# Kernel optimization log

Measured on AMD Instinct MI355X. Metric: run time of the kernel, lower is better.

Reference implementation:

```python
import jax, jax.numpy as jnp
import numpy as np

B, N_AIM, N_DET, C = 4, 2048, 2048, 256  # inplanes=256, inter_channels=128


def _lin(x, w, b):
    # torch nn.Linear: y = x @ W^T + b, weight shape [out, in]
    return jnp.einsum('bnc,dc->bnd', x, w) + b


def setup_inputs() -> dict:
    key = jax.random.key(0)
    ks = jax.random.split(key, 16)
    s = 1.0 / np.sqrt(C)
    inp = {
        'detect': jax.random.normal(ks[0], (B, N_DET, C), jnp.float32),
        'aim': jax.random.normal(ks[1], (B, N_AIM, C), jnp.float32),
    }
    names = ['g', 'g2', 'theta', 'phi', 'W', 'Q']
    for i, nm in enumerate(names):
        inp[nm + '_w'] = jax.random.uniform(ks[2 + 2 * i], (C, C), jnp.float32, -s, s)
        inp[nm + '_b'] = jax.random.uniform(ks[3 + 2 * i], (C,), jnp.float32, -s, s)
    return inp


def reference(detect, aim, g_w, g_b, g2_w, g2_b, theta_w, theta_b, phi_w, phi_b, W_w, W_b, Q_w, Q_b):
    b, na, c = aim.shape
    nd = detect.shape[1]
    ic = c // 2  # inter_channels

    # view(B, ic, -1) on a contiguous [B, N, C] tensor -> row-major reshape to [B, ic, 2N]
    d_x = _lin(detect, g_w, g_b).reshape(b, ic, -1).transpose(0, 2, 1)      # (B, 2Nd, ic)
    a_x = _lin(aim, g2_w, g2_b).reshape(b, ic, -1).transpose(0, 2, 1)       # (B, 2Na, ic)
    theta_x = _lin(aim, theta_w, theta_b).reshape(b, ic, -1).transpose(0, 2, 1)  # (B, 2Na, ic)
    phi_x = _lin(detect, phi_w, phi_b).reshape(b, ic, -1)                   # (B, ic, 2Nd)

    f = jnp.matmul(theta_x, phi_x)                 # (B, 2Na, 2Nd)
    f_div_C = f / f.shape[-1]                      # scale by 2*Nd
    fi_div_C = jnp.swapaxes(f, 1, 2) / f.shape[-2] # (B, 2Nd, 2Na), scale by 2*Na

    non_aim = jnp.matmul(f_div_C, d_x)             # (B, 2Na, ic)
    non_aim = non_aim.transpose(0, 2, 1).reshape(b, na, c)
    non_aim = _lin(non_aim, W_w, W_b) + aim

    non_det = jnp.matmul(fi_div_C, a_x)            # (B, 2Nd, ic)
    non_det = non_det.transpose(0, 2, 1).reshape(b, nd, c)
    non_det = _lin(non_det, Q_w, Q_b) + detect

    return (non_det, non_aim)
```

## Files before the change

### kernel.cpp

```cpp
#include <hip/hip_runtime.h>


typedef __attribute__((ext_vector_type(4))) float  f32x4;
typedef __attribute__((ext_vector_type(8))) __bf16 bf16x8;
typedef __attribute__((ext_vector_type(8))) unsigned short u16x8;
typedef __attribute__((ext_vector_type(4))) unsigned short u16x4;

__device__ inline unsigned short f2bf(float f) {
    union { float f; unsigned u; } c; c.f = f;
    unsigned r = c.u + 0x7FFF + ((c.u >> 16) & 1);
    return (unsigned short)(r >> 16);
}
__device__ inline bf16x8 ldfrag(const unsigned short* p) {
    return __builtin_bit_cast(bf16x8, *(const u16x8*)p);
}

struct Params {
    const float *detect, *aim;
    const float *g_w, *g2_w, *th_w, *ph_w, *W_w, *Q_w;
    const float *g_b, *g2_b, *th_b, *ph_b, *W_b, *Q_b;
    unsigned short *Wbf;
    unsigned short *T, *P, *Gd, *Ga;
    float *Spart;
    float *out_det, *out_aim;
};

__global__ __launch_bounds__(256)
void linall_kernel(Params p)
{
    const int z = blockIdx.z, set = blockIdx.x;
    const float* A  = z ? p.detect : p.aim;
    const float* Wm = z ? (set ? p.g_w : p.ph_w) : (set ? p.g2_w : p.th_w);
    const float* Bv = z ? (set ? p.g_b : p.ph_b) : (set ? p.g2_b : p.th_b);
    unsigned short* O = z ? (set ? p.Gd : p.P) : (set ? p.Ga : p.T);
    const int m0 = blockIdx.y * 128;

    __shared__ unsigned short As[128][40];
    __shared__ unsigned short Bs[256][40];

    const int tid = threadIdx.x, lane = tid & 63, w = tid >> 6;
    const int wr = w >> 1, wc = w & 1, q = lane >> 4, ln = lane & 15;

    f32x4 acc[4][8] = {};

    for (int k0 = 0; k0 < 256; k0 += 32) {
        #pragma unroll
        for (int i = 0; i < 4; ++i) {
            int c = tid + i * 256, row = c >> 3, c4 = c & 7;
            float4 v = *((const float4*)(A + (size_t)(m0 + row) * 256 + k0) + c4);
            u16x4 pk; pk[0]=f2bf(v.x); pk[1]=f2bf(v.y); pk[2]=f2bf(v.z); pk[3]=f2bf(v.w);
            *(u16x4*)&As[row][c4 * 4] = pk;
        }
        #pragma unroll
        for (int i = 0; i < 8; ++i) {
            int c = tid + i * 256, row = c >> 3, c4 = c & 7;
            float4 v = *((const float4*)(Wm + (size_t)row * 256 + k0) + c4);
            u16x4 pk; pk[0]=f2bf(v.x); pk[1]=f2bf(v.y); pk[2]=f2bf(v.z); pk[3]=f2bf(v.w);
            *(u16x4*)&Bs[row][c4 * 4] = pk;
        }
        __syncthreads();
        bf16x8 af[4], bb[8];
        #pragma unroll
        for (int i = 0; i < 4; ++i) af[i] = ldfrag(&As[wr * 64 + i * 16 + ln][q * 8]);
        #pragma unroll
        for (int j = 0; j < 8; ++j) bb[j] = ldfrag(&Bs[wc * 128 + j * 16 + ln][q * 8]);
        #pragma unroll
        for (int i = 0; i < 4; ++i)
            #pragma unroll
            for (int j = 0; j < 8; ++j)
                acc[i][j] = __builtin_amdgcn_mfma_f32_16x16x32_bf16(af[i], bb[j], acc[i][j], 0, 0, 0);
        __syncthreads();
    }

    #pragma unroll
    for (int i = 0; i < 4; ++i)
        #pragma unroll
        for (int j = 0; j < 8; ++j) {
            int n = wc * 128 + j * 16 + ln;
            float bias = Bv[n];
            #pragma unroll
            for (int r = 0; r < 4; ++r) {
                int m = m0 + wr * 64 + i * 16 + q * 4 + r;
                O[(size_t)m * 256 + n] = f2bf(acc[i][j][r] + bias);
            }
        }
}

__global__ __launch_bounds__(256)
void spart_kernel(Params p)
{
    const int bx = blockIdx.x, tid = threadIdx.x;

    if (tid < 128) {
        int fi = bx * 128 + tid;
        const float* src = fi < 16384 ? p.W_w : p.Q_w;
        float4 v = ((const float4*)src)[fi & 16383];
        u16x4 pk; pk[0]=f2bf(v.x); pk[1]=f2bf(v.y); pk[2]=f2bf(v.z); pk[3]=f2bf(v.w);
        ((u16x4*)p.Wbf)[fi] = pk;
    }

    const int which = bx >> 7, batch = (bx >> 5) & 3, ms = (bx >> 4) & 1, chunk = bx & 15;
    const unsigned short* A = (which ? p.Ga : p.Gd) + (size_t)batch * 524288;
    const unsigned short* B = (which ? p.T  : p.P ) + (size_t)batch * 524288;
    float* Sp = p.Spart + ((size_t)(which * 4 + batch) * 16 + chunk) * 16384;
    const int kbeg = chunk * 256;

    __shared__ unsigned short As[64][72], Bs[128][72];
    const int lane = tid & 63, w = tid >> 6;
    const int wr = w >> 1, wc = w & 1, q = lane >> 4, ln = lane & 15;

    f32x4 acc[2][4] = {};

    for (int st = 0; st < 4; ++st) {
        const int k0 = kbeg + st * 64;
        #pragma unroll
        for (int i = 0; i < 2; ++i) {
            int c = tid + i * 256, row = c >> 3, c8 = c & 7;
            *(u16x8*)&As[row][c8 * 8] =
                *(const u16x8*)(A + (size_t)(ms * 64 + row) * 4096 + k0 + c8 * 8);
        }
        #pragma unroll
        for (int i = 0; i < 4; ++i) {
            int c = tid + i * 256, row = c >> 3, c8 = c & 7;
            *(u16x8*)&Bs[row][c8 * 8] = *(const u16x8*)(B + (size_t)row * 4096 + k0 + c8 * 8);
        }
        __syncthreads();
        #pragma unroll
        for (int ks = 0; ks < 2; ++ks) {
            bf16x8 af[2], bb[4];
            #pragma unroll
            for (int i = 0; i < 2; ++i) af[i] = ldfrag(&As[wr * 32 + i * 16 + ln][ks * 32 + q * 8]);
            #pragma unroll
            for (int j = 0; j < 4; ++j) bb[j] = ldfrag(&Bs[wc * 64 + j * 16 + ln][ks * 32 + q * 8]);
            #pragma unroll
            for (int i = 0; i < 2; ++i)
                #pragma unroll
                for (int j = 0; j < 4; ++j)
                    acc[i][j] = __builtin_amdgcn_mfma_f32_16x16x32_bf16(af[i], bb[j], acc[i][j], 0, 0, 0);
        }
        __syncthreads();
    }

    #pragma unroll
    for (int i = 0; i < 2; ++i)
        #pragma unroll
        for (int j = 0; j < 4; ++j)
            #pragma unroll
            for (int r = 0; r < 4; ++r) {
                int m = ms * 64 + wr * 32 + i * 16 + q * 4 + r;
                int n = wc * 64 + j * 16 + ln;
                Sp[m * 128 + n] = acc[i][j][r];
            }
}

__global__ __launch_bounds__(256)
void outfused_kernel(Params p)
{
    const int bx = blockIdx.x, tid = threadIdx.x;
    const int lane = tid & 63, w = tid >> 6;
    const int wr = w >> 1, wc = w & 1, q = lane >> 4, ln = lane & 15;

    const int which = bx >> 8, batch = (bx >> 6) & 3, s = (bx >> 2) & 15, mq = bx & 3;
    const int m0 = mq * 32;
    const float* SpG = p.Spart + ((size_t)(which * 4 + batch) * 16) * 16384;
    const unsigned short* X = (which ? p.P : p.T) + (size_t)batch * 524288;
    const unsigned short* Wm = p.Wbf + (which ? 65536 : 0);
    const float* Bv = which ? p.Q_b : p.W_b;
    const float* R  = which ? p.detect : p.aim;
    float* O = which ? p.out_det : p.out_aim;

    __shared__ union {
        struct { unsigned short Ss[32][136]; unsigned short Xs[32][268]; } g1;
        struct { unsigned short NAs[32][268]; unsigned short Ws[256][40]; } g2;
    } sm;

    #pragma unroll
    for (int it = 0; it < 4; ++it) {
        int fi = tid + it * 256;
        int mi = fi >> 5, k4 = fi & 31;
        const float* base = SpG + (size_t)(m0 + mi) * 128 + k4 * 4;
        f32x4 sum = {};
        #pragma unroll
        for (int c = 0; c < 16; ++c)
            sum += *(const f32x4*)(base + (size_t)c * 16384);
        u16x4 pk; pk[0]=f2bf(sum[0]); pk[1]=f2bf(sum[1]); pk[2]=f2bf(sum[2]); pk[3]=f2bf(sum[3]);
        *(u16x4*)&sm.g1.Ss[mi][k4 * 4] = pk;
    }
    __syncthreads();

    f32x4 acc1[8] = {};
    for (int kc = 0; kc < 4; ++kc) {
        const int k0 = kc * 32;
        #pragma unroll
        for (int i = 0; i < 4; ++i) {
            int c = tid + i * 256, kk = c >> 5, j8 = c & 31;
            u16x8 v = *(const u16x8*)(X + (size_t)(k0 + kk) * 4096 + s * 256 + j8 * 8);
            u16x4 lo, hi;
            lo[0]=v[0]; lo[1]=v[1]; lo[2]=v[2]; lo[3]=v[3];
            hi[0]=v[4]; hi[1]=v[5]; hi[2]=v[6]; hi[3]=v[7];
            *(u16x4*)&sm.g1.Xs[kk][j8 * 8]     = lo;
            *(u16x4*)&sm.g1.Xs[kk][j8 * 8 + 4] = hi;
        }
        __syncthreads();
        bf16x8 af = ldfrag(&sm.g1.Ss[wr * 16 + ln][kc * 32 + q * 8]);
        #pragma unroll
        for (int nt = 0; nt < 8; ++nt) {
            int col = wc * 128 + nt * 16 + ln;
            u16x8 t;
            #pragma unroll
            for (int i = 0; i < 8; ++i) t[i] = sm.g1.Xs[q * 8 + i][col];
            acc1[nt] = __builtin_amdgcn_mfma_f32_16x16x32_bf16(
                af, __builtin_bit_cast(bf16x8, t), acc1[nt], 0, 0, 0);
        }
        __syncthreads();
    }

    #pragma unroll
    for (int nt = 0; nt < 8; ++nt)
        #pragma unroll
        for (int r = 0; r < 4; ++r) {
            int mi = wr * 16 + q * 4 + r;
            int jj = wc * 128 + nt * 16 + ln;
            sm.g2.NAs[mi][jj] = f2bf(acc1[nt][r] * (1.0f / 4096.0f));
        }
    __syncthreads();

    f32x4 acc2[8] = {};
    for (int cc = 0; cc < 8; ++cc) {
        const int c0 = cc * 32;
        #pragma unroll
        for (int i = 0; i < 4; ++i) {
            int c = tid + i * 256, row = c >> 2, c8 = c & 3;
            *(u16x8*)&sm.g2.Ws[row][c8 * 8] =
                *(const u16x8*)(Wm + (size_t)row * 256 + c0 + c8 * 8);
        }
        __syncthreads();
        u16x8 t;
        #pragma unroll
        for (int i = 0; i < 8; ++i) t[i] = sm.g2.NAs[wr * 16 + ln][c0 + q * 8 + i];
        bf16x8 af = __builtin_bit_cast(bf16x8, t);
        #pragma unroll
        for (int nt = 0; nt < 8; ++nt) {
            bf16x8 bb = ldfrag(&sm.g2.Ws[wc * 128 + nt * 16 + ln][q * 8]);
            acc2[nt] = __builtin_amdgcn_mfma_f32_16x16x32_bf16(af, bb, acc2[nt], 0, 0, 0);
        }
        __syncthreads();
    }

    #pragma unroll
    for (int nt = 0; nt < 8; ++nt) {
        int n = wc * 128 + nt * 16 + ln;
        float bias = Bv[n];
        #pragma unroll
        for (int r = 0; r < 4; ++r) {
            int mi = wr * 16 + q * 4 + r;
            int row = (m0 + mi) * 16 + s;
            size_t idx = ((size_t)batch * 2048 + row) * 256 + n;
            O[idx] = acc2[nt][r] + bias + R[idx];
        }
    }
}

extern "C" void kernel_launch(void* const* d_in, const int* in_sizes, int n_in,
                              void* d_out, int out_size, void* d_ws, size_t ws_size,
                              hipStream_t stream)
{
    Params p;
    p.detect = (const float*)d_in[0];
    p.aim    = (const float*)d_in[1];
    p.g_w  = (const float*)d_in[2];  p.g_b  = (const float*)d_in[3];
    p.g2_w = (const float*)d_in[4];  p.g2_b = (const float*)d_in[5];
    p.th_w = (const float*)d_in[6];  p.th_b = (const float*)d_in[7];
    p.ph_w = (const float*)d_in[8];  p.ph_b = (const float*)d_in[9];
    p.W_w  = (const float*)d_in[10]; p.W_b  = (const float*)d_in[11];
    p.Q_w  = (const float*)d_in[12]; p.Q_b  = (const float*)d_in[13];

    const size_t TOT = 8192L * 256;

    unsigned short* ws16 = (unsigned short*)d_ws;
    p.Wbf = ws16;
    p.T   = p.Wbf + 2 * 65536;
    p.P   = p.T  + TOT;
    p.Gd  = p.P  + TOT;
    p.Ga  = p.Gd + TOT;
    p.Spart = (float*)(p.Ga + TOT);

    p.out_det = (float*)d_out;
    p.out_aim = p.out_det + TOT;

    linall_kernel<<<dim3(2, 64, 2), 256, 0, stream>>>(p);
    spart_kernel<<<dim3(256), 256, 0, stream>>>(p);
    outfused_kernel<<<dim3(512), 256, 0, stream>>>(p);
}
```

Baseline: 161.3 us.

## Fold output projection into input weights and split pipeline into five kernels

Precomputes W·theta_w and Q·phi_w (plus folded biases) so the final output GEMM runs directly against precomputed Z projections, removing the second fused GEMM stage. Inputs and weights are pre-converted to bf16 in a separate pass, the projection GEMM now produces six outputs with smaller tiles, and the split-K partial reduction moves into its own kernel. The aim is more parallelism and less per-block work, at the cost of extra launches, an extra projection GEMM and more workspace traffic. The weights composed in bf16 also change rounding.

```diff
diff --git a/kernel.cpp b/kernel.cpp
--- a/kernel.cpp
+++ b/kernel.cpp
@@ -19,246 +19,265 @@
     const float *detect, *aim;
     const float *g_w, *g2_w, *th_w, *ph_w, *W_w, *Q_w;
     const float *g_b, *g2_b, *th_b, *ph_b, *W_b, *Q_b;
-    unsigned short *Wbf;
-    unsigned short *T, *P, *Gd, *Ga;
+    unsigned short *Wall;
+    unsigned short *Abf, *Dbf;
+    unsigned short *T, *Ga, *Za, *P, *Gd, *Zd;
+    unsigned short *S;
     float *Spart;
+    float *bc;
     float *out_det, *out_aim;
 };
 
 __global__ __launch_bounds__(256)
-void linall_kernel(Params p)
-{
-    const int z = blockIdx.z, set = blockIdx.x;
-    const float* A  = z ? p.detect : p.aim;
-    const float* Wm = z ? (set ? p.g_w : p.ph_w) : (set ? p.g2_w : p.th_w);
-    const float* Bv = z ? (set ? p.g_b : p.ph_b) : (set ? p.g2_b : p.th_b);
-    unsigned short* O = z ? (set ? p.Gd : p.P) : (set ? p.Ga : p.T);
-    const int m0 = blockIdx.y * 128;
-
-    __shared__ unsigned short As[128][40];
-    __shared__ unsigned short Bs[256][40];
+void wcomp_kernel(Params p)
+{
+    const int bx = blockIdx.x, tid = threadIdx.x;
+    if (bx < 32) {
+        const int comp = bx >> 4, r0 = (bx & 15) * 16;
+        const float* Wbig = comp ? p.Q_w : p.W_w;
+        const float* Th   = comp ? p.ph_w : p.th_w;
+        const float* tb   = comp ? p.ph_b : p.th_b;
+        unsigned short* out = p.Wall + (size_t)(comp ? 5 : 2) * 65536;
+        float* bco = p.bc + comp * 256;
+
+        __shared__ float Wl[16][257];
+        __shared__ float red[16][17];
+        #pragma unroll
+        for (int i = 0; i < 16; ++i)
+            Wl[i][tid] = Wbig[(size_t)(r0 + i) * 256 + tid];
+        __syncthreads();
+
+        float acc[16] = {};
+        for (int c = 0; c < 256; ++c) {
+            float th = Th[(size_t)c * 256 + tid];
+            #pragma unroll
+            for (int i = 0; i < 16; ++i) acc[i] += Wl[i][c] * th;
+        }
+        #pragma unroll
+        for (int i = 0; i < 16; ++i)
+            out[(size_t)(r0 + i) * 256 + tid] = f2bf(acc[i]);
+
+        {
+            int i = tid >> 4, c0 = (tid & 15) * 16;
+            float s = 0.f;
+            #pragma unroll
+            for (int c = 0; c < 16; ++c) s += Wl[i][c0 + c] * tb[c0 + c];
+            red[i][tid & 15] = s;
+        }
+        __syncthreads();
+        if (tid < 16) {
+            float s = 0.f;
+            #pragma unroll
+            for (int j = 0; j < 16; ++j) s += red[tid][j];
+            bco[r0 + tid] = s;
+        }
+    } else {
+        const size_t stride = 64 * 256;
+        for (size_t t = (size_t)(bx - 32) * 256 + tid; t < 1114112; t += stride) {
+            const float* src; unsigned short* dst; size_t off;
+            if (t < 524288)       { src = p.aim;    dst = p.Abf;              off = t; }
+            else if (t < 1048576) { src = p.detect; dst = p.Dbf;              off = t - 524288; }
+            else if (t < 1064960) { src = p.th_w;   dst = p.Wall;             off = t - 1048576; }
+            else if (t < 1081344) { src = p.g2_w;   dst = p.Wall + 65536;     off = t - 1064960; }
+            else if (t < 1097728) { src = p.ph_w;   dst = p.Wall + 3 * 65536; off = t - 1081344; }
+            else                  { src = p.g_w;    dst = p.Wall + 4 * 65536; off = t - 1097728; }
+            float4 v = ((const float4*)src)[off];
+            u16x4 pk; pk[0]=f2bf(v.x); pk[1]=f2bf(v.y); pk[2]=f2bf(v.z); pk[3]=f2bf(v.w);
+            ((u16x4*)dst)[off] = pk;
+        }
+    }
+}
+
+__global__ __launch_bounds__(256, 4)
+void linall6_kernel(Params p)
+{
+    const int combo = blockIdx.z;
+    const unsigned short* A = combo < 3 ? p.Abf : p.Dbf;
+    const unsigned short* Wm = p.Wall + (size_t)combo * 65536;
+    const float* Bv; unsigned short* O;
+    switch (combo) {
+        case 0:  Bv = p.th_b;     O = p.T;  break;
+        case 1:  Bv = p.g2_b;     O = p.Ga; break;
+        case 2:  Bv = p.bc;       O = p.Za; break;
+        case 3:  Bv = p.ph_b;     O = p.P;  break;
+        case 4:  Bv = p.g_b;      O = p.Gd; break;
+        default: Bv = p.bc + 256; O = p.Zd; break;
+    }
+    const int m0 = blockIdx.y * 64, n0 = blockIdx.x * 128;
+
+    __shared__ unsigned short As[64][40];
+    __shared__ unsigned short Bs[128][40];
 
     const int tid = threadIdx.x, lane = tid & 63, w = tid >> 6;
     const int wr = w >> 1, wc = w & 1, q = lane >> 4, ln = lane & 15;
 
-    f32x4 acc[4][8] = {};
+    f32x4 acc[2][4] = {};
 
     for (int k0 = 0; k0 < 256; k0 += 32) {
-        #pragma unroll
-        for (int i = 0; i < 4; ++i) {
-            int c = tid + i * 256, row = c >> 3, c4 = c & 7;
-            float4 v = *((const float4*)(A + (size_t)(m0 + row) * 256 + k0) + c4);
-            u16x4 pk; pk[0]=f2bf(v.x); pk[1]=f2bf(v.y); pk[2]=f2bf(v.z); pk[3]=f2bf(v.w);
-            *(u16x4*)&As[row][c4 * 4] = pk;
-        }
-        #pragma unroll
-        for (int i = 0; i < 8; ++i) {
-            int c = tid + i * 256, row = c >> 3, c4 = c & 7;
-            float4 v = *((const float4*)(Wm + (size_t)row * 256 + k0) + c4);
-            u16x4 pk; pk[0]=f2bf(v.x); pk[1]=f2bf(v.y); pk[2]=f2bf(v.z); pk[3]=f2bf(v.w);
-            *(u16x4*)&Bs[row][c4 * 4] = pk;
-        }
-        __syncthreads();
-        bf16x8 af[4], bb[8];
-        #pragma unroll
-        for (int i = 0; i < 4; ++i) af[i] = ldfrag(&As[wr * 64 + i * 16 + ln][q * 8]);
-        #pragma unroll
-        for (int j = 0; j < 8; ++j) bb[j] = ldfrag(&Bs[wc * 128 + j * 16 + ln][q * 8]);
-        #pragma unroll
-        for (int i = 0; i < 4; ++i)
-            #pragma unroll
-            for (int j = 0; j < 8; ++j)
+        {
+            int row = tid >> 2, c8 = tid & 3;
+            *(u16x8*)&As[row][c8 * 8] = *(const u16x8*)(A + (size_t)(m0 + row) * 256 + k0 + c8 * 8);
+        }
+        #pragma unroll
+        for (int i = 0; i < 2; ++i) {
+            int c = tid + i * 256, row = c >> 2, c8 = c & 3;
+            *(u16x8*)&Bs[row][c8 * 8] = *(const u16x8*)(Wm + (size_t)(n0 + row) * 256 + k0 + c8 * 8);
+        }
+        __syncthreads();
+        bf16x8 af[2], bb[4];
+        #pragma unroll
+        for (int i = 0; i < 2; ++i) af[i] = ldfrag(&As[wr * 32 + i * 16 + ln][q * 8]);
+        #pragma unroll
+        for (int j = 0; j < 4; ++j) bb[j] = ldfrag(&Bs[wc * 64 + j * 16 + ln][q * 8]);
+        #pragma unroll
+        for (int i = 0; i < 2; ++i)
+            #pragma unroll
+            for (int j = 0; j < 4; ++j)
                 acc[i][j] = __builtin_amdgcn_mfma_f32_16x16x32_bf16(af[i], bb[j], acc[i][j], 0, 0, 0);
         __syncthreads();
     }
 
     #pragma unroll
-    for (int i = 0; i < 4; ++i)
-        #pragma unroll
-        for (int j = 0; j < 8; ++j) {
-            int n = wc * 128 + j * 16 + ln;
+    for (int i = 0; i < 2; ++i)
+        #pragma unroll
+        for (int j = 0; j < 4; ++j) {
+            int n = n0 + wc * 64 + j * 16 + ln;
             float bias = Bv[n];
             #pragma unroll
             for (int r = 0; r < 4; ++r) {
-                int m = m0 + wr * 64 + i * 16 + q * 4 + r;
+                int m = m0 + wr * 32 + i * 16 + q * 4 + r;
                 O[(size_t)m * 256 + n] = f2bf(acc[i][j][r] + bias);
             }
         }
 }
 
-__global__ __launch_bounds__(256)
+__global__ __launch_bounds__(256, 4)
 void spart_kernel(Params p)
 {
     const int bx = blockIdx.x, tid = threadIdx.x;
-
-    if (tid < 128) {
-        int fi = bx * 128 + tid;
-        const float* src = fi < 16384 ? p.W_w : p.Q_w;
-        float4 v = ((const float4*)src)[fi & 16383];
-        u16x4 pk; pk[0]=f2bf(v.x); pk[1]=f2bf(v.y); pk[2]=f2bf(v.z); pk[3]=f2bf(v.w);
-        ((u16x4*)p.Wbf)[fi] = pk;
-    }
-
-    const int which = bx >> 7, batch = (bx >> 5) & 3, ms = (bx >> 4) & 1, chunk = bx & 15;
+    const int which = bx >> 8, batch = (bx >> 6) & 3;
+    const int ms = (bx >> 5) & 1, ns = (bx >> 4) & 1, chunk = bx & 15;
     const unsigned short* A = (which ? p.Ga : p.Gd) + (size_t)batch * 524288;
     const unsigned short* B = (which ? p.T  : p.P ) + (size_t)batch * 524288;
     float* Sp = p.Spart + ((size_t)(which * 4 + batch) * 16 + chunk) * 16384;
     const int kbeg = chunk * 256;
 
-    __shared__ unsigned short As[64][72], Bs[128][72];
+    __shared__ unsigned short As[64][40], Bs[64][40];
     const int lane = tid & 63, w = tid >> 6;
     const int wr = w >> 1, wc = w & 1, q = lane >> 4, ln = lane & 15;
 
-    f32x4 acc[2][4] = {};
-
-    for (int st = 0; st < 4; ++st) {
-        const int k0 = kbeg + st * 64;
-        #pragma unroll
-        for (int i = 0; i < 2; ++i) {
-            int c = tid + i * 256, row = c >> 3, c8 = c & 7;
+    f32x4 acc[2][2] = {};
+
+    for (int k0 = kbeg; k0 < kbeg + 256; k0 += 32) {
+        {
+            int row = tid >> 2, c8 = tid & 3;
             *(u16x8*)&As[row][c8 * 8] =
                 *(const u16x8*)(A + (size_t)(ms * 64 + row) * 4096 + k0 + c8 * 8);
-        }
-        #pragma unroll
-        for (int i = 0; i < 4; ++i) {
-            int c = tid + i * 256, row = c >> 3, c8 = c & 7;
-            *(u16x8*)&Bs[row][c8 * 8] = *(const u16x8*)(B + (size_t)row * 4096 + k0 + c8 * 8);
-        }
-        __syncthreads();
-        #pragma unroll
-        for (int ks = 0; ks < 2; ++ks) {
-            bf16x8 af[2], bb[4];
-            #pragma unroll
-            for (int i = 0; i < 2; ++i) af[i] = ldfrag(&As[wr * 32 + i * 16 + ln][ks * 32 + q * 8]);
-            #pragma unroll
-            for (int j = 0; j < 4; ++j) bb[j] = ldfrag(&Bs[wc * 64 + j * 16 + ln][ks * 32 + q * 8]);
-            #pragma unroll
-            for (int i = 0; i < 2; ++i)
-                #pragma unroll
-                for (int j = 0; j < 4; ++j)
-                    acc[i][j] = __builtin_amdgcn_mfma_f32_16x16x32_bf16(af[i], bb[j], acc[i][j], 0, 0, 0);
-        }
+            *(u16x8*)&Bs[row][c8 * 8] =
+                *(const u16x8*)(B + (size_t)(ns * 64 + row) * 4096 + k0 + c8 * 8);
+        }
+        __syncthreads();
+        bf16x8 af[2], bb[2];
+        #pragma unroll
+        for (int i = 0; i < 2; ++i) af[i] = ldfrag(&As[wr * 32 + i * 16 + ln][q * 8]);
+        #pragma unroll
+        for (int j = 0; j < 2; ++j) bb[j] = ldfrag(&Bs[wc * 32 + j * 16 + ln][q * 8]);
+        #pragma unroll
+        for (int i = 0; i < 2; ++i)
+            #pragma unroll
+            for (int j = 0; j < 2; ++j)
+                acc[i][j] = __builtin_amdgcn_mfma_f32_16x16x32_bf16(af[i], bb[j], acc[i][j], 0, 0, 0);
         __syncthreads();
     }
 
     #pragma unroll
     for (int i = 0; i < 2; ++i)
         #pragma unroll
-        for (int j = 0; j < 4; ++j)
+        for (int j = 0; j < 2; ++j)
             #pragma unroll
             for (int r = 0; r < 4; ++r) {
                 int m = ms * 64 + wr * 32 + i * 16 + q * 4 + r;
-                int n = wc * 64 + j * 16 + ln;
+                int n = ns * 64 + wc * 32 + j * 16 + ln;
                 Sp[m * 128 + n] = acc[i][j][r];
             }
 }
 
 __global__ __launch_bounds__(256)
-void outfused_kernel(Params p)
+void sred_kernel(Params p)
+{
+    const int fi = blockIdx.x * 256 + threadIdx.x;
+    const int g = fi >> 12, e4 = fi & 4095;
+    const float* base = p.Spart + (size_t)g * 16 * 16384 + (size_t)e4 * 4;
+    f32x4 s = {};
+    #pragma unroll
+    for (int c = 0; c < 16; ++c) s += *(const f32x4*)(base + (size_t)c * 16384);
+    u16x4 pk; pk[0]=f2bf(s[0]); pk[1]=f2bf(s[1]); pk[2]=f2bf(s[2]); pk[3]=f2bf(s[3]);
+    *(u16x4*)(p.S + (size_t)g * 16384 + e4 * 4) = pk;
+}
+
+__global__ __launch_bounds__(256, 4)
+void outgemm_kernel(Params p)
 {
     const int bx = blockIdx.x, tid = threadIdx.x;
     const int lane = tid & 63, w = tid >> 6;
-    const int wr = w >> 1, wc = w & 1, q = lane >> 4, ln = lane & 15;
-
-    const int which = bx >> 8, batch = (bx >> 6) & 3, s = (bx >> 2) & 15, mq = bx & 3;
-    const int m0 = mq * 32;
-    const float* SpG = p.Spart + ((size_t)(which * 4 + batch) * 16) * 16384;
-    const unsigned short* X = (which ? p.P : p.T) + (size_t)batch * 524288;
-    const unsigned short* Wm = p.Wbf + (which ? 65536 : 0);
+    const int q = lane >> 4, ln = lane & 15;
+
+    const int which = bx >> 9, batch = (bx >> 7) & 3, mt = (bx >> 5) & 3, nt4 = bx & 31;
+    const int m0 = mt * 32, n0 = nt4 * 128;
+    const unsigned short* Sg = p.S + (size_t)(which * 4 + batch) * 16384 + (size_t)m0 * 128;
+    const unsigned short* Z = (which ? p.Zd : p.Za) + (size_t)batch * 524288;
     const float* Bv = which ? p.Q_b : p.W_b;
     const float* R  = which ? p.detect : p.aim;
     float* O = which ? p.out_det : p.out_aim;
-
-    __shared__ union {
-        struct { unsigned short Ss[32][136]; unsigned short Xs[32][268]; } g1;
-        struct { unsigned short NAs[32][268]; unsigned short Ws[256][40]; } g2;
-    } sm;
-
-    #pragma unroll
-    for (int it = 0; it < 4; ++it) {
-        int fi = tid + it * 256;
-        int mi = fi >> 5, k4 = fi & 31;
-        const float* base = SpG + (size_t)(m0 + mi) * 128 + k4 * 4;
-        f32x4 sum = {};
-        #pragma unroll
-        for (int c = 0; c < 16; ++c)
-            sum += *(const f32x4*)(base + (size_t)c * 16384);
-        u16x4 pk; pk[0]=f2bf(sum[0]); pk[1]=f2bf(sum[1]); pk[2]=f2bf(sum[2]); pk[3]=f2bf(sum[3]);
-        *(u16x4*)&sm.g1.Ss[mi][k4 * 4] = pk;
-    }
-    __syncthreads();
-
-    f32x4 acc1[8] = {};
+    const int s = n0 >> 8, cbase = n0 & 255;
+
+    __shared__ unsigned short Zs[32][136];
+
+    bf16x8 af[4][2];
+    #pragma unroll
+    for (int kc = 0; kc < 4; ++kc)
+        #pragma unroll
+        for (int mi = 0; mi < 2; ++mi)
+            af[kc][mi] = ldfrag(Sg + (size_t)(mi * 16 + ln) * 128 + kc * 32 + q * 8);
+
+    f32x4 acc[2][2] = {};
     for (int kc = 0; kc < 4; ++kc) {
-        const int k0 = kc * 32;
-        #pragma unroll
-        for (int i = 0; i < 4; ++i) {
-            int c = tid + i * 256, kk = c >> 5, j8 = c & 31;
-            u16x8 v = *(const u16x8*)(X + (size_t)(k0 + kk) * 4096 + s * 256 + j8 * 8);
-            u16x4 lo, hi;
-            lo[0]=v[0]; lo[1]=v[1]; lo[2]=v[2]; lo[3]=v[3];
-            hi[0]=v[4]; hi[1]=v[5]; hi[2]=v[6]; hi[3]=v[7];
-            *(u16x4*)&sm.g1.Xs[kk][j8 * 8]     = lo;
-            *(u16x4*)&sm.g1.Xs[kk][j8 * 8 + 4] = hi;
-        }
-        __syncthreads();
-        bf16x8 af = ldfrag(&sm.g1.Ss[wr * 16 + ln][kc * 32 + q * 8]);
-        #pragma unroll
-        for (int nt = 0; nt < 8; ++nt) {
-            int col = wc * 128 + nt * 16 + ln;
+        #pragma unroll
+        for (int it = 0; it < 2; ++it) {
+            int c = tid + it * 256, kk = c >> 4, j8 = c & 15;
+            *(u16x8*)&Zs[kk][j8 * 8] =
+                *(const u16x8*)(Z + (size_t)(kc * 32 + kk) * 4096 + n0 + j8 * 8);
+        }
+        __syncthreads();
+        #pragma unroll
+        for (int ntl = 0; ntl < 2; ++ntl) {
+            int col = w * 32 + ntl * 16 + ln;
             u16x8 t;
             #pragma unroll
-            for (int i = 0; i < 8; ++i) t[i] = sm.g1.Xs[q * 8 + i][col];
-            acc1[nt] = __builtin_amdgcn_mfma_f32_16x16x32_bf16(
-                af, __builtin_bit_cast(bf16x8, t), acc1[nt], 0, 0, 0);
-        }
-        __syncthreads();
-    }
-
-    #pragma unroll
-    for (int nt = 0; nt < 8; ++nt)
-        #pragma unroll
-        for (int r = 0; r < 4; ++r) {
-            int mi = wr * 16 + q * 4 + r;
-            int jj = wc * 128 + nt * 16 + ln;
-            sm.g2.NAs[mi][jj] = f2bf(acc1[nt][r] * (1.0f / 4096.0f));
-        }
-    __syncthreads();
-
-    f32x4 acc2[8] = {};
-    for (int cc = 0; cc < 8; ++cc) {
-        const int c0 = cc * 32;
-        #pragma unroll
-        for (int i = 0; i < 4; ++i) {
-            int c = tid + i * 256, row = c >> 2, c8 = c & 3;
-            *(u16x8*)&sm.g2.Ws[row][c8 * 8] =
-                *(const u16x8*)(Wm + (size_t)row * 256 + c0 + c8 * 8);
-        }
-        __syncthreads();
-        u16x8 t;
-        #pragma unroll
-        for (int i = 0; i < 8; ++i) t[i] = sm.g2.NAs[wr * 16 + ln][c0 + q * 8 + i];
-        bf16x8 af = __builtin_bit_cast(bf16x8, t);
-        #pragma unroll
-        for (int nt = 0; nt < 8; ++nt) {
-            bf16x8 bb = ldfrag(&sm.g2.Ws[wc * 128 + nt * 16 + ln][q * 8]);
-            acc2[nt] = __builtin_amdgcn_mfma_f32_16x16x32_bf16(af, bb, acc2[nt], 0, 0, 0);
-        }
-        __syncthreads();
-    }
-
-    #pragma unroll
-    for (int nt = 0; nt < 8; ++nt) {
-        int n = wc * 128 + nt * 16 + ln;
-        float bias = Bv[n];
-        #pragma unroll
-        for (int r = 0; r < 4; ++r) {
-            int mi = wr * 16 + q * 4 + r;
-            int row = (m0 + mi) * 16 + s;
-            size_t idx = ((size_t)batch * 2048 + row) * 256 + n;
-            O[idx] = acc2[nt][r] + bias + R[idx];
-        }
-    }
+            for (int i = 0; i < 8; ++i) t[i] = Zs[q * 8 + i][col];
+            bf16x8 bb = __builtin_bit_cast(bf16x8, t);
+            #pragma unroll
+            for (int mi = 0; mi < 2; ++mi)
+                acc[mi][ntl] = __builtin_amdgcn_mfma_f32_16x16x32_bf16(af[kc][mi], bb, acc[mi][ntl], 0, 0, 0);
+        }
+        __syncthreads();
+    }
+
+    #pragma unroll
+    for (int mi = 0; mi < 2; ++mi)
+        #pragma unroll
+        for (int ntl = 0; ntl < 2; ++ntl) {
+            int jl = w * 32 + ntl * 16 + ln;
+            int c = cbase + jl;
+            float bias = Bv[c];
+            #pragma unroll
+            for (int r = 0; r < 4; ++r) {
+                int mv = m0 + mi * 16 + q * 4 + r;
+                int row = mv * 16 + s;
+                size_t idx = ((size_t)batch * 2048 + row) * 256 + c;
+                O[idx] = acc[mi][ntl][r] * (1.0f / 4096.0f) + bias + R[idx];
+            }
+        }
 }
 
 extern "C" void kernel_launch(void* const* d_in, const int* in_sizes, int n_in,
@@ -278,17 +297,25 @@
     const size_t TOT = 8192L * 256;
 
     unsigned short* ws16 = (unsigned short*)d_ws;
-    p.Wbf = ws16;
-    p.T   = p.Wbf + 2 * 65536;
-    p.P   = p.T  + TOT;
-    p.Gd  = p.P  + TOT;
-    p.Ga  = p.Gd + TOT;
-    p.Spart = (float*)(p.Ga + TOT);
+    p.Wall = ws16;
+    p.Abf  = p.Wall + 6 * 65536;
+    p.Dbf  = p.Abf + TOT;
+    p.T    = p.Dbf + TOT;
+    p.Ga   = p.T  + TOT;
+    p.Za   = p.Ga + TOT;
+    p.P    = p.Za + TOT;
+    p.Gd   = p.P  + TOT;
+    p.Zd   = p.Gd + TOT;
+    p.S    = p.Zd + TOT;
+    p.Spart = (float*)(p.S + 8 * 16384);
+    p.bc    = p.Spart + 8 * 16 * 16384;
 
     p.out_det = (float*)d_out;
     p.out_aim = p.out_det + TOT;
 
-    linall_kernel<<<dim3(2, 64, 2), 256, 0, stream>>>(p);
-    spart_kernel<<<dim3(256), 256, 0, stream>>>(p);
-    outfused_kernel<<<dim3(512), 256, 0, stream>>>(p);
-}
+    wcomp_kernel  <<<96, 256, 0, stream>>>(p);
+    linall6_kernel<<<dim3(2, 128, 6), 256, 0, stream>>>(p);
+    spart_kernel  <<<512, 256, 0, stream>>>(p);
+    sred_kernel   <<<128, 256, 0, stream>>>(p);
+    outgemm_kernel<<<1024, 256, 0, stream>>>(p);
+}
```

New measurement: 162.6 us. No clear change (+0.8%).
